# Kernel optimization log

Measured on AMD Instinct MI355X. Metric: run time of the kernel, lower is better.

Reference implementation:

```python
import jax, jax.numpy as jnp
import numpy as np

# ----- problem dimensions (must match setup_inputs) -----
B = 50          # graphs per batch
NPG = 2000      # nodes per graph (equal-size graphs)
N = B * NPG     # total nodes = 100_000
D = 128         # in_channels
E = 600_000     # total edges
EA = 16         # edge_attr_dim
RATIO = 0.5
K = int(RATIO * NPG)  # nodes kept per graph = 1000
EPS = 1e-6


def setup_inputs() -> dict:
    key = jax.random.key(0)
    ks = jax.random.split(key, 12)
    x = jax.random.normal(ks[0], (N, D), jnp.float32)
    # edges constrained within graphs (each graph owns a contiguous node block)
    eg = jax.random.randint(ks[1], (E,), 0, B)
    src = eg * NPG + jax.random.randint(ks[2], (E,), 0, NPG)
    dst = eg * NPG + jax.random.randint(ks[3], (E,), 0, NPG)
    edge_index = jnp.stack([src, dst]).astype(jnp.int32)
    edge_attr = jax.random.normal(ks[4], (E, EA), jnp.float32)
    batch = (jnp.arange(N) // NPG).astype(jnp.int32)
    # feat_mlp: Linear(D,D) -> ReLU -> Linear(D,1)
    W1 = jax.random.normal(ks[5], (D, D), jnp.float32) / np.sqrt(D)
    b1 = jnp.zeros((D,), jnp.float32)
    W2 = jax.random.normal(ks[6], (D, 1), jnp.float32) / np.sqrt(D)
    b2 = jnp.zeros((1,), jnp.float32)
    # edge_mlp: Linear(EA,D) -> ReLU -> Linear(D,1)
    We1 = jax.random.normal(ks[7], (EA, D), jnp.float32) / np.sqrt(EA)
    be1 = jnp.zeros((D,), jnp.float32)
    We2 = jax.random.normal(ks[8], (D, 1), jnp.float32) / np.sqrt(D)
    be2 = jnp.zeros((1,), jnp.float32)
    view_weight = jnp.ones((3,), jnp.float32)
    return {"x": x, "edge_index": edge_index, "edge_attr": edge_attr,
            "batch": batch, "W1": W1, "b1": b1, "W2": W2, "b2": b2,
            "We1": We1, "be1": be1, "We2": We2, "be2": be2,
            "view_weight": view_weight}


def _standardize(v):
    # torch .std() is unbiased (ddof=1)
    return (v - v.mean()) / (jnp.std(v, ddof=1) + EPS)


def _scores(x, src, dst, edge_attr, W1, b1, W2, b2, We1, be1, We2, be2, vw):
    # edge weights: softplus(edge_mlp(edge_attr)) + eps
    ew = jax.nn.softplus((jax.nn.relu(edge_attr @ We1 + be1) @ We2 + be2)[:, 0]) + EPS
    deg_w = jnp.zeros((N,), x.dtype).at[src].add(ew)
    dis = jnp.where(deg_w > 0, deg_w ** -0.5, 0.0)
    norm = dis[src] * ew * dis[dst]                       # [E]
    x_diff = jnp.zeros_like(x).at[src].add(x[dst] * norm[:, None])  # [N,D]
    # view 1: structural (log degree)
    deg_c = jnp.zeros((N,), x.dtype).at[src].add(1.0)
    struct_score = _standardize(jnp.log(deg_c + 1.0))
    # view 2: feature MLP
    feat_raw = (jax.nn.relu(x @ W1 + b1) @ W2 + b2)[:, 0]
    feat_score = _standardize(feat_raw)
    # view 3: diffusion cosine similarity
    dot = jnp.sum(x * x_diff, axis=-1)
    cos = dot / ((jnp.linalg.norm(x, axis=-1) + EPS) *
                 (jnp.linalg.norm(x_diff, axis=-1) + EPS))
    diff_score = _standardize(cos)
    raw = jnp.stack([struct_score, feat_score, diff_score], axis=-1) @ vw
    return jax.nn.sigmoid(raw)                            # [N]


def reference(x, edge_index, edge_attr, batch, W1, b1, W2, b2,
              We1, be1, We2, be2, view_weight):
    src, dst = edge_index[0], edge_index[1]
    score = _scores(x, src, dst, edge_attr, W1, b1, W2, b2,
                    We1, be1, We2, be2, view_weight)
    # vectorized per-graph top-k (graphs are equal-size contiguous blocks)
    loc = jax.lax.top_k(score.reshape(B, NPG), K)[1]      # [B,K] local indices
    keep = (jnp.arange(B, dtype=loc.dtype)[:, None] * NPG + loc).reshape(-1)  # [B*K]
    node_mask = jnp.zeros((N,), bool).at[keep].set(True)
    new_id = jnp.full((N,), -1, jnp.int32).at[keep].set(
        jnp.arange(B * K, dtype=jnp.int32))
    e_mask = node_mask[src] & node_mask[dst]              # [E]
    out_edge_index = jnp.where(e_mask[None, :],
                               jnp.stack([new_id[src], new_id[dst]]), 0)
    out_edge_attr = jnp.where(e_mask[:, None], edge_attr, 0.0)
    out_x = x[keep] * score[keep][:, None]                # [B*K, D]
    out_batch = (jnp.arange(B * K) // K).astype(batch.dtype)
    return out_x, out_edge_index, out_edge_attr, out_batch, e_mask
```

## Files before the change

kernel.cpp:

```cpp
#include <hip/hip_runtime.h>
#include <math.h>

#define NN   100000
#define DD   128
#define EE   600000
#define EAD  16
#define BB   50
#define NPG  2000
#define KK   1000
#define NKEEP (BB*KK)

#define OFF_OEI    6400000
#define OFF_OEA    7600000
#define OFF_OBATCH 17200000
#define OFF_EMASK  17250000

#define NRED 240
#define SCAN_NB 98

__global__ __launch_bounds__(256) void k_edge_mlp(
    const float* __restrict__ edge_attr, const int* __restrict__ src,
    const float* __restrict__ We1, const float* __restrict__ be1,
    const float* __restrict__ We2, const float* __restrict__ be2,
    float* __restrict__ ew, float* __restrict__ deg_w, float* __restrict__ deg_c)
{
    int e = blockIdx.x * 256 + threadIdx.x;
    if (e >= EE) return;
    const float4* ap = (const float4*)(edge_attr + (size_t)e * EAD);
    float4 a0 = ap[0], a1 = ap[1], a2 = ap[2], a3 = ap[3];
    float ea[16] = {a0.x,a0.y,a0.z,a0.w, a1.x,a1.y,a1.z,a1.w,
                    a2.x,a2.y,a2.z,a2.w, a3.x,a3.y,a3.z,a3.w};
    float acc = be2[0];
    for (int j = 0; j < DD; j++) {
        float h = be1[j];
        #pragma unroll
        for (int k = 0; k < 16; k++) h += ea[k] * We1[k*DD + j];
        acc += fmaxf(h, 0.f) * We2[j];
    }
    float sp = fmaxf(acc, 0.f) + log1pf(expf(-fabsf(acc)));
    float w = sp + 1e-6f;
    ew[e] = w;
    int s = src[e];
    atomicAdd(&deg_w[s], w);
    atomicAdd(&deg_c[s], 1.0f);
}

__global__ __launch_bounds__(256) void k_dis(const float* __restrict__ deg_w,
                                             float* __restrict__ dis)
{
    int n = blockIdx.x * 256 + threadIdx.x;
    if (n >= NN) return;
    float d = deg_w[n];
    dis[n] = d > 0.f ? 1.f / sqrtf(d) : 0.f;
}

__global__ __launch_bounds__(1024) void k_scan_block(
    const float* __restrict__ deg_c, int* __restrict__ scanned,
    int* __restrict__ blocksums)
{
    __shared__ int s[1024];
    int i = blockIdx.x * 1024 + threadIdx.x;
    int c = (i < NN) ? (int)deg_c[i] : 0;
    s[threadIdx.x] = c;
    __syncthreads();
    for (int off = 1; off < 1024; off <<= 1) {
        int v = (threadIdx.x >= off) ? s[threadIdx.x - off] : 0;
        __syncthreads();
        s[threadIdx.x] += v;
        __syncthreads();
    }
    if (i < NN) scanned[i] = s[threadIdx.x] - c;
    if (threadIdx.x == 1023) blocksums[blockIdx.x] = s[1023];
}

__global__ __launch_bounds__(128) void k_scan_top(int* __restrict__ blocksums)
{
    __shared__ int s[128];
    int c = (threadIdx.x < SCAN_NB) ? blocksums[threadIdx.x] : 0;
    s[threadIdx.x] = c;
    __syncthreads();
    for (int off = 1; off < 128; off <<= 1) {
        int v = (threadIdx.x >= off) ? s[threadIdx.x - off] : 0;
        __syncthreads();
        s[threadIdx.x] += v;
        __syncthreads();
    }
    if (threadIdx.x < SCAN_NB) blocksums[threadIdx.x] = s[threadIdx.x] - c;
}

__global__ __launch_bounds__(256) void k_cursor(
    const int* __restrict__ scanned, const int* __restrict__ blocksums,
    int* __restrict__ rowstart, int* __restrict__ cur)
{
    int n = blockIdx.x * 256 + threadIdx.x;
    if (n >= NN) return;
    int st = scanned[n] + blocksums[n >> 10];
    rowstart[n] = st;
    cur[n] = st;
}

__global__ __launch_bounds__(256) void k_scatter(
    const int* __restrict__ src, const int* __restrict__ dst,
    const float* __restrict__ ew, const float* __restrict__ dis,
    int* __restrict__ cur, int* __restrict__ csr_dst, float* __restrict__ csr_w)
{
    int e = blockIdx.x * 256 + threadIdx.x;
    if (e >= EE) return;
    int s = src[e], d = dst[e];
    float w = dis[s] * ew[e] * dis[d];
    int pos = atomicAdd(&cur[s], 1);
    csr_dst[pos] = d;
    csr_w[pos] = w;
}

__global__ __launch_bounds__(256) void k_gather(
    const int* __restrict__ rowstart, const float* __restrict__ deg_c,
    const int* __restrict__ csr_dst, const float* __restrict__ csr_w,
    const float* __restrict__ x, float* __restrict__ x_diff)
{
    int wid = (blockIdx.x * 256 + threadIdx.x) >> 6;
    int lane = threadIdx.x & 63;
    if (wid >= NN) return;
    int start = rowstart[wid];
    int end = start + (int)deg_c[wid];
    const float2* xp = (const float2*)x;
    float2 acc = {0.f, 0.f};
    for (int e = start; e < end; e++) {
        int d = csr_dst[e];
        float w = csr_w[e];
        float2 xv = xp[(size_t)d * 64 + lane];
        acc.x += xv.x * w;
        acc.y += xv.y * w;
    }
    ((float2*)x_diff)[(size_t)wid * 64 + lane] = acc;
}

#define XSTR 132
__global__ __launch_bounds__(256) void k_node(
    const float* __restrict__ x, const float* __restrict__ x_diff,
    const float* __restrict__ W1, const float* __restrict__ b1,
    const float* __restrict__ W2, const float* __restrict__ b2,
    const float* __restrict__ deg_c,
    float* __restrict__ raw0, float* __restrict__ raw1, float* __restrict__ raw2)
{
    __shared__ float xs[64 * XSTR];
    int wave = threadIdx.x >> 6, lane = threadIdx.x & 63;
    int ng = lane >> 4, jg = lane & 15;
    int blockBase = blockIdx.x * 64;

    #pragma unroll
    for (int it = 0; it < 8; it++) {
        int s = threadIdx.x + 256 * it;
        int row = s >> 5, c4 = s & 31;
        int gn = blockBase + row; if (gn >= NN) gn = NN - 1;
        *(float4*)(xs + row * XSTR + c4 * 4) =
            *(const float4*)(x + (size_t)gn * DD + c4 * 4);
    }
    __syncthreads();

    const float* xw = xs + (wave * 16 + ng * 4) * XSTR;
    int j0 = jg * 8;
    float acc[4][8];
    #pragma unroll
    for (int i = 0; i < 4; i++)
        #pragma unroll
        for (int jj = 0; jj < 8; jj++) acc[i][jj] = 0.f;

    for (int k = 0; k < DD; k += 4) {
        float4 xv[4];
        #pragma unroll
        for (int i = 0; i < 4; i++) xv[i] = *(const float4*)(xw + i * XSTR + k);
        float4 wv[4][2];
        #pragma unroll
        for (int kk = 0; kk < 4; kk++) {
            wv[kk][0] = *(const float4*)(W1 + (k + kk) * DD + j0);
            wv[kk][1] = *(const float4*)(W1 + (k + kk) * DD + j0 + 4);
        }
        #pragma unroll
        for (int i = 0; i < 4; i++) {
            const float xe[4] = {xv[i].x, xv[i].y, xv[i].z, xv[i].w};
            #pragma unroll
            for (int kk = 0; kk < 4; kk++) {
                acc[i][0] += xe[kk] * wv[kk][0].x;
                acc[i][1] += xe[kk] * wv[kk][0].y;
                acc[i][2] += xe[kk] * wv[kk][0].z;
                acc[i][3] += xe[kk] * wv[kk][0].w;
                acc[i][4] += xe[kk] * wv[kk][1].x;
                acc[i][5] += xe[kk] * wv[kk][1].y;
                acc[i][6] += xe[kk] * wv[kk][1].z;
                acc[i][7] += xe[kk] * wv[kk][1].w;
            }
        }
    }

    float4 b1a = *(const float4*)(b1 + j0), b1b = *(const float4*)(b1 + j0 + 4);
    float4 w2a = *(const float4*)(W2 + j0), w2b = *(const float4*)(W2 + j0 + 4);
    const float b1v[8] = {b1a.x,b1a.y,b1a.z,b1a.w, b1b.x,b1b.y,b1b.z,b1b.w};
    const float w2v[8] = {w2a.x,w2a.y,w2a.z,w2a.w, w2b.x,w2b.y,w2b.z,w2b.w};
    float bias2 = b2[0];
    #pragma unroll
    for (int i = 0; i < 4; i++) {
        float p = 0.f;
        #pragma unroll
        for (int jj = 0; jj < 8; jj++)
            p += fmaxf(acc[i][jj] + b1v[jj], 0.f) * w2v[jj];
        p += __shfl_xor(p, 1, 64);
        p += __shfl_xor(p, 2, 64);
        p += __shfl_xor(p, 4, 64);
        p += __shfl_xor(p, 8, 64);
        int node = blockBase + wave * 16 + ng * 4 + i;
        if (jg == 0 && node < NN) raw1[node] = p + bias2;
    }

    const float* xwv = xs + wave * 16 * XSTR;
    #pragma unroll 1
    for (int nd = 0; nd < 16; nd++) {
        int node = blockBase + wave * 16 + nd;
        int rn = node < NN ? node : NN - 1;
        float2 xv2 = *(const float2*)(xwv + nd * XSTR + lane * 2);
        float2 xd2 = *(const float2*)(x_diff + (size_t)rn * DD + lane * 2);
        float dot = xv2.x * xd2.x + xv2.y * xd2.y;
        float nx  = xv2.x * xv2.x + xv2.y * xv2.y;
        float ndn = xd2.x * xd2.x + xd2.y * xd2.y;
        #pragma unroll
        for (int off = 32; off; off >>= 1) {
            dot += __shfl_xor(dot, off, 64);
            nx  += __shfl_xor(nx,  off, 64);
            ndn += __shfl_xor(ndn, off, 64);
        }
        if (lane == 0 && node < NN)
            raw2[node] = dot / ((sqrtf(nx) + 1e-6f) * (sqrtf(ndn) + 1e-6f));
    }
    if (lane < 16) {
        int node = blockBase + wave * 16 + lane;
        if (node < NN) raw0[node] = logf(deg_c[node] + 1.0f);
    }
}

__global__ __launch_bounds__(256) void k_reduce(
    const float* __restrict__ r0, const float* __restrict__ r1,
    const float* __restrict__ r2, double* __restrict__ partials)
{
    __shared__ double sd[256];
    double s[6] = {0,0,0,0,0,0};
    for (int n = blockIdx.x * 256 + threadIdx.x; n < NN; n += 256 * NRED) {
        double v0 = r0[n], v1 = r1[n], v2 = r2[n];
        s[0] += v0; s[1] += v0*v0;
        s[2] += v1; s[3] += v1*v1;
        s[4] += v2; s[5] += v2*v2;
    }
    for (int q = 0; q < 6; q++) {
        sd[threadIdx.x] = s[q];
        __syncthreads();
        for (int off = 128; off; off >>= 1) {
            if (threadIdx.x < off) sd[threadIdx.x] += sd[threadIdx.x + off];
            __syncthreads();
        }
        if (threadIdx.x == 0) partials[blockIdx.x * 6 + q] = sd[0];
        __syncthreads();
    }
}

__global__ __launch_bounds__(256) void k_stats(const double* __restrict__ partials,
                                               float* __restrict__ stats)
{
    __shared__ double sd[256];
    __shared__ double sums[6];
    for (int q = 0; q < 6; q++) {
        sd[threadIdx.x] = (threadIdx.x < NRED) ? partials[threadIdx.x * 6 + q] : 0.0;
        __syncthreads();
        for (int off = 128; off; off >>= 1) {
            if (threadIdx.x < off) sd[threadIdx.x] += sd[threadIdx.x + off];
            __syncthreads();
        }
        if (threadIdx.x == 0) sums[q] = sd[0];
        __syncthreads();
    }
    if (threadIdx.x == 0) {
        for (int i = 0; i < 3; i++) {
            double sum = sums[2*i], sq = sums[2*i+1];
            double mean = sum / NN;
            double var = (sq - sum * sum / NN) / (NN - 1);
            double sdv = sqrt(var > 0 ? var : 0);
            stats[2*i]   = (float)mean;
            stats[2*i+1] = (float)(1.0 / (sdv + 1e-6));
        }
    }
}

__global__ __launch_bounds__(256) void k_score(
    const float* __restrict__ r0, const float* __restrict__ r1,
    const float* __restrict__ r2, const float* __restrict__ stats,
    const float* __restrict__ vw, float* __restrict__ score)
{
    int n = blockIdx.x * 256 + threadIdx.x;
    if (n >= NN) return;
    float z0 = (r0[n] - stats[0]) * stats[1];
    float z1 = (r1[n] - stats[2]) * stats[3];
    float z2 = (r2[n] - stats[4]) * stats[5];
    float r = z0 * vw[0] + z1 * vw[1] + z2 * vw[2];
    score[n] = 1.f / (1.f + expf(-r));
}

__global__ __launch_bounds__(1024) void k_topk(
    const float* __restrict__ score, int* __restrict__ keep,
    int* __restrict__ new_id, float* __restrict__ obatch)
{
    __shared__ unsigned long long keys[2048];
    int b = blockIdx.x;
    unsigned t = threadIdx.x;
    for (unsigned i = t; i < 2048; i += 1024) {
        unsigned long long kk = 0ull;
        if (i < NPG) {
            float sc = score[b * NPG + i];
            kk = ((unsigned long long)__float_as_uint(sc) << 32)
               | (unsigned long long)(0xFFFFFFFFu - i);
        }
        keys[i] = kk;
    }
    __syncthreads();
    for (unsigned k = 2; k <= 2048; k <<= 1) {
        for (unsigned j = k >> 1; j > 0; j >>= 1) {
            unsigned i = ((t & ~(j - 1)) << 1) | (t & (j - 1));
            unsigned p = i | j;
            unsigned long long a = keys[i], c = keys[p];
            bool up = ((i & k) == 0);
            if ((a < c) == up) { keys[i] = c; keys[p] = a; }
            __syncthreads();
        }
    }
    if (t < KK) {
        unsigned long long kk = keys[t];
        unsigned li = 0xFFFFFFFFu - (unsigned)(kk & 0xFFFFFFFFu);
        int node = b * NPG + (int)li;
        int j = b * KK + (int)t;
        keep[j] = node;
        new_id[node] = j;
        obatch[j] = (float)b;
    }
}

__global__ __launch_bounds__(128) void k_outx(
    const float* __restrict__ x, const float* __restrict__ score,
    const int* __restrict__ keep, float* __restrict__ out_x)
{
    int j = blockIdx.x;
    int node = keep[j];
    float s = score[node];
    out_x[(size_t)j * DD + threadIdx.x] = x[(size_t)node * DD + threadIdx.x] * s;
}

__global__ __launch_bounds__(256) void k_edges(
    const int* __restrict__ src, const int* __restrict__ dst,
    const int* __restrict__ new_id, float* __restrict__ oei,
    float* __restrict__ emask)
{
    int e = blockIdx.x * 256 + threadIdx.x;
    if (e >= EE) return;
    int ns = new_id[src[e]], nd = new_id[dst[e]];
    bool m = (ns >= 0) && (nd >= 0);
    oei[e]      = m ? (float)ns : 0.f;
    oei[EE + e] = m ? (float)nd : 0.f;
    emask[e]    = m ? 1.f : 0.f;
}

__global__ __launch_bounds__(256) void k_attr(
    const float* __restrict__ edge_attr, const float* __restrict__ emask,
    float* __restrict__ oea)
{
    int idx = blockIdx.x * 256 + threadIdx.x;
    if (idx >= EE * 4) return;
    int e = idx >> 2;
    float m = emask[e];
    float4 v = ((const float4*)edge_attr)[idx];
    float4 o; o.x = v.x*m; o.y = v.y*m; o.z = v.z*m; o.w = v.w*m;
    ((float4*)oea)[idx] = o;
}

extern "C" void kernel_launch(void* const* d_in, const int* in_sizes, int n_in,
                              void* d_out, int out_size, void* d_ws, size_t ws_size,
                              hipStream_t stream) {
    const float* x         = (const float*)d_in[0];
    const int*   edge_idx  = (const int*)d_in[1];
    const float* edge_attr = (const float*)d_in[2];
    const float* W1  = (const float*)d_in[4];
    const float* b1  = (const float*)d_in[5];
    const float* W2  = (const float*)d_in[6];
    const float* b2  = (const float*)d_in[7];
    const float* We1 = (const float*)d_in[8];
    const float* be1 = (const float*)d_in[9];
    const float* We2 = (const float*)d_in[10];
    const float* be2 = (const float*)d_in[11];
    const float* vw  = (const float*)d_in[12];

    const int* src = edge_idx;
    const int* dst = edge_idx + EE;

    float* out    = (float*)d_out;
    float* out_x  = out;
    float* oei    = out + OFF_OEI;
    float* oea    = out + OFF_OEA;
    float* obatch = out + OFF_OBATCH;
    float* emask  = out + OFF_EMASK;

    float* x_diff    = out;
    int*   csr_dst   = (int*)(out + 12800000);
    float* csr_w     = out + 13400000;
    int*   rowstart  = (int*)(out + 14000000);
    int*   cur       = (int*)(out + 14100000);
    int*   scanned   = (int*)(out + 14200000);
    int*   blocksums = (int*)(out + 14300000);

    float* ws     = (float*)d_ws;
    float* ew     = ws;
    float* deg_w  = ws + 600000;
    float* deg_c  = ws + 700000;
    float* dis    = ws + 800000;
    float* score  = ws + 900000;
    float* raw0   = ws + 1000000;
    float* raw1   = ws + 1100000;
    float* raw2   = ws + 1200000;
    int*   keep   = (int*)(ws + 1300000);
    int*   new_id = (int*)(ws + 1350000);
    double* partials = (double*)(ws + 1450000);
    float* stats  = ws + 1450000 + 2 * 6 * NRED;

    hipMemsetAsync(deg_w, 0, 2 * NN * sizeof(float), stream);
    hipMemsetAsync(new_id, 0xFF, NN * sizeof(int), stream);

    k_edge_mlp<<<(EE + 255) / 256, 256, 0, stream>>>(edge_attr, src, We1, be1, We2, be2,
                                                     ew, deg_w, deg_c);
    k_dis<<<(NN + 255) / 256, 256, 0, stream>>>(deg_w, dis);
    k_scan_block<<<SCAN_NB, 1024, 0, stream>>>(deg_c, scanned, blocksums);
    k_scan_top<<<1, 128, 0, stream>>>(blocksums);
    k_cursor<<<(NN + 255) / 256, 256, 0, stream>>>(scanned, blocksums, rowstart, cur);
    k_scatter<<<(EE + 255) / 256, 256, 0, stream>>>(src, dst, ew, dis, cur, csr_dst, csr_w);
    k_gather<<<(NN * 64 + 255) / 256, 256, 0, stream>>>(rowstart, deg_c, csr_dst, csr_w,
                                                        x, x_diff);
    k_node<<<(NN + 63) / 64, 256, 0, stream>>>(x, x_diff, W1, b1, W2, b2, deg_c,
                                               raw0, raw1, raw2);
    k_reduce<<<NRED, 256, 0, stream>>>(raw0, raw1, raw2, partials);
    k_stats<<<1, 256, 0, stream>>>(partials, stats);
    k_score<<<(NN + 255) / 256, 256, 0, stream>>>(raw0, raw1, raw2, stats, vw, score);
    k_topk<<<BB, 1024, 0, stream>>>(score, keep, new_id, obatch);
    k_outx<<<NKEEP, 128, 0, stream>>>(x, score, keep, out_x);
    k_edges<<<(EE + 255) / 256, 256, 0, stream>>>(src, dst, new_id, oei, emask);
    k_attr<<<(EE * 4 + 255) / 256, 256, 0, stream>>>(edge_attr, emask, oea);
}
```

Measured before the change: 512.5 us.

## Fuse cosine similarity into neighbor gather and tile edge MLP weights in LDS

The edge MLP kernel now stages a transposed copy of We1, be1 and We2 in shared memory and has each thread process four edges, reusing each weight load across them. The neighbor gather now computes the cosine-similarity and log-degree features directly, so the x_diff array is never written to memory or read back in the node kernel. The gather also loads CSR indices and weights cooperatively across the wavefront and broadcasts them with shuffles, unrolled four at a time for more memory parallelism. The edge kernel gains register pressure and launches fewer blocks.

```diff
diff --git a/kernel.cpp b/kernel.cpp
--- a/kernel.cpp
+++ b/kernel.cpp
@@ -18,31 +18,73 @@
 #define NRED 240
 #define SCAN_NB 98
 
+#define EPB 1024
 __global__ __launch_bounds__(256) void k_edge_mlp(
     const float* __restrict__ edge_attr, const int* __restrict__ src,
     const float* __restrict__ We1, const float* __restrict__ be1,
     const float* __restrict__ We2, const float* __restrict__ be2,
     float* __restrict__ ew, float* __restrict__ deg_w, float* __restrict__ deg_c)
 {
-    int e = blockIdx.x * 256 + threadIdx.x;
-    if (e >= EE) return;
-    const float4* ap = (const float4*)(edge_attr + (size_t)e * EAD);
-    float4 a0 = ap[0], a1 = ap[1], a2 = ap[2], a3 = ap[3];
-    float ea[16] = {a0.x,a0.y,a0.z,a0.w, a1.x,a1.y,a1.z,a1.w,
-                    a2.x,a2.y,a2.z,a2.w, a3.x,a3.y,a3.z,a3.w};
-    float acc = be2[0];
+    __shared__ float wt[2048];
+    __shared__ float b1s[128];
+    __shared__ float w2s[128];
+    for (int idx = threadIdx.x; idx < 2048; idx += 256) {
+        int j = idx >> 4, k = idx & 15;
+        wt[idx] = We1[k * DD + j];
+    }
+    if (threadIdx.x < 128) {
+        b1s[threadIdx.x] = be1[threadIdx.x];
+        w2s[threadIdx.x] = We2[threadIdx.x];
+    }
+    __syncthreads();
+
+    int e0 = blockIdx.x * EPB + threadIdx.x;
+    float ea[4][16];
+    #pragma unroll
+    for (int i = 0; i < 4; i++) {
+        int e = e0 + 256 * i; if (e >= EE) e = EE - 1;
+        const float4* ap = (const float4*)(edge_attr + (size_t)e * EAD);
+        float4 a0 = ap[0], a1 = ap[1], a2 = ap[2], a3 = ap[3];
+        ea[i][0]=a0.x; ea[i][1]=a0.y; ea[i][2]=a0.z; ea[i][3]=a0.w;
+        ea[i][4]=a1.x; ea[i][5]=a1.y; ea[i][6]=a1.z; ea[i][7]=a1.w;
+        ea[i][8]=a2.x; ea[i][9]=a2.y; ea[i][10]=a2.z; ea[i][11]=a2.w;
+        ea[i][12]=a3.x; ea[i][13]=a3.y; ea[i][14]=a3.z; ea[i][15]=a3.w;
+    }
+    float acc[4] = {0.f, 0.f, 0.f, 0.f};
     for (int j = 0; j < DD; j++) {
-        float h = be1[j];
-        #pragma unroll
-        for (int k = 0; k < 16; k++) h += ea[k] * We1[k*DD + j];
-        acc += fmaxf(h, 0.f) * We2[j];
-    }
-    float sp = fmaxf(acc, 0.f) + log1pf(expf(-fabsf(acc)));
-    float w = sp + 1e-6f;
-    ew[e] = w;
-    int s = src[e];
-    atomicAdd(&deg_w[s], w);
-    atomicAdd(&deg_c[s], 1.0f);
+        float4 w0 = *(const float4*)(wt + j*16);
+        float4 w1 = *(const float4*)(wt + j*16 + 4);
+        float4 w2 = *(const float4*)(wt + j*16 + 8);
+        float4 w3 = *(const float4*)(wt + j*16 + 12);
+        float bj = b1s[j], w2j = w2s[j];
+        #pragma unroll
+        for (int i = 0; i < 4; i++) {
+            float h = bj;
+            h += ea[i][0]*w0.x;  h += ea[i][1]*w0.y;
+            h += ea[i][2]*w0.z;  h += ea[i][3]*w0.w;
+            h += ea[i][4]*w1.x;  h += ea[i][5]*w1.y;
+            h += ea[i][6]*w1.z;  h += ea[i][7]*w1.w;
+            h += ea[i][8]*w2.x;  h += ea[i][9]*w2.y;
+            h += ea[i][10]*w2.z; h += ea[i][11]*w2.w;
+            h += ea[i][12]*w3.x; h += ea[i][13]*w3.y;
+            h += ea[i][14]*w3.z; h += ea[i][15]*w3.w;
+            acc[i] += fmaxf(h, 0.f) * w2j;
+        }
+    }
+    float bias2 = be2[0];
+    #pragma unroll
+    for (int i = 0; i < 4; i++) {
+        int e = e0 + 256 * i;
+        if (e < EE) {
+            float a = acc[i] + bias2;
+            float sp = fmaxf(a, 0.f) + log1pf(expf(-fabsf(a)));
+            float w = sp + 1e-6f;
+            ew[e] = w;
+            int s = src[e];
+            atomicAdd(&deg_w[s], w);
+            atomicAdd(&deg_c[s], 1.0f);
+        }
+    }
 }
 
 __global__ __launch_bounds__(256) void k_dis(const float* __restrict__ deg_w,
@@ -113,35 +155,69 @@
     csr_w[pos] = w;
 }
 
-__global__ __launch_bounds__(256) void k_gather(
+__global__ __launch_bounds__(256) void k_gather_cos(
     const int* __restrict__ rowstart, const float* __restrict__ deg_c,
     const int* __restrict__ csr_dst, const float* __restrict__ csr_w,
-    const float* __restrict__ x, float* __restrict__ x_diff)
-{
-    int wid = (blockIdx.x * 256 + threadIdx.x) >> 6;
+    const float* __restrict__ x, float* __restrict__ raw0, float* __restrict__ raw2)
+{
+    int node = (blockIdx.x * 256 + threadIdx.x) >> 6;
     int lane = threadIdx.x & 63;
-    if (wid >= NN) return;
-    int start = rowstart[wid];
-    int end = start + (int)deg_c[wid];
+    if (node >= NN) return;
+    int start = rowstart[node];
+    int deg = (int)deg_c[node];
     const float2* xp = (const float2*)x;
+    float2 xn = xp[(size_t)node * 64 + lane];
     float2 acc = {0.f, 0.f};
-    for (int e = start; e < end; e++) {
-        int d = csr_dst[e];
-        float w = csr_w[e];
-        float2 xv = xp[(size_t)d * 64 + lane];
-        acc.x += xv.x * w;
-        acc.y += xv.y * w;
-    }
-    ((float2*)x_diff)[(size_t)wid * 64 + lane] = acc;
+    for (int base = 0; base < deg; base += 64) {
+        int rem = deg - base; if (rem > 64) rem = 64;
+        int md = 0; float mw = 0.f;
+        if (lane < rem) {
+            md = csr_dst[start + base + lane];
+            mw = csr_w[start + base + lane];
+        }
+        int e = 0;
+        for (; e + 4 <= rem; e += 4) {
+            int d0 = __shfl(md, e, 64),   d1 = __shfl(md, e+1, 64);
+            int d2 = __shfl(md, e+2, 64), d3 = __shfl(md, e+3, 64);
+            float w0 = __shfl(mw, e, 64),   w1 = __shfl(mw, e+1, 64);
+            float w2 = __shfl(mw, e+2, 64), w3 = __shfl(mw, e+3, 64);
+            float2 v0 = xp[(size_t)d0 * 64 + lane];
+            float2 v1 = xp[(size_t)d1 * 64 + lane];
+            float2 v2 = xp[(size_t)d2 * 64 + lane];
+            float2 v3 = xp[(size_t)d3 * 64 + lane];
+            acc.x += w0 * v0.x; acc.y += w0 * v0.y;
+            acc.x += w1 * v1.x; acc.y += w1 * v1.y;
+            acc.x += w2 * v2.x; acc.y += w2 * v2.y;
+            acc.x += w3 * v3.x; acc.y += w3 * v3.y;
+        }
+        for (; e < rem; e++) {
+            int d = __shfl(md, e, 64);
+            float w = __shfl(mw, e, 64);
+            float2 v = xp[(size_t)d * 64 + lane];
+            acc.x += w * v.x; acc.y += w * v.y;
+        }
+    }
+    float dot = xn.x * acc.x + xn.y * acc.y;
+    float nx  = xn.x * xn.x + xn.y * xn.y;
+    float nd  = acc.x * acc.x + acc.y * acc.y;
+    #pragma unroll
+    for (int off = 32; off; off >>= 1) {
+        dot += __shfl_xor(dot, off, 64);
+        nx  += __shfl_xor(nx,  off, 64);
+        nd  += __shfl_xor(nd,  off, 64);
+    }
+    if (lane == 0) {
+        raw2[node] = dot / ((sqrtf(nx) + 1e-6f) * (sqrtf(nd) + 1e-6f));
+        raw0[node] = logf((float)deg + 1.0f);
+    }
 }
 
 #define XSTR 132
 __global__ __launch_bounds__(256) void k_node(
-    const float* __restrict__ x, const float* __restrict__ x_diff,
+    const float* __restrict__ x,
     const float* __restrict__ W1, const float* __restrict__ b1,
     const float* __restrict__ W2, const float* __restrict__ b2,
-    const float* __restrict__ deg_c,
-    float* __restrict__ raw0, float* __restrict__ raw1, float* __restrict__ raw2)
+    float* __restrict__ raw1)
 {
     __shared__ float xs[64 * XSTR];
     int wave = threadIdx.x >> 6, lane = threadIdx.x & 63;
@@ -210,30 +286,6 @@
         p += __shfl_xor(p, 8, 64);
         int node = blockBase + wave * 16 + ng * 4 + i;
         if (jg == 0 && node < NN) raw1[node] = p + bias2;
-    }
-
-    const float* xwv = xs + wave * 16 * XSTR;
-    #pragma unroll 1
-    for (int nd = 0; nd < 16; nd++) {
-        int node = blockBase + wave * 16 + nd;
-        int rn = node < NN ? node : NN - 1;
-        float2 xv2 = *(const float2*)(xwv + nd * XSTR + lane * 2);
-        float2 xd2 = *(const float2*)(x_diff + (size_t)rn * DD + lane * 2);
-        float dot = xv2.x * xd2.x + xv2.y * xd2.y;
-        float nx  = xv2.x * xv2.x + xv2.y * xv2.y;
-        float ndn = xd2.x * xd2.x + xd2.y * xd2.y;
-        #pragma unroll
-        for (int off = 32; off; off >>= 1) {
-            dot += __shfl_xor(dot, off, 64);
-            nx  += __shfl_xor(nx,  off, 64);
-            ndn += __shfl_xor(ndn, off, 64);
-        }
-        if (lane == 0 && node < NN)
-            raw2[node] = dot / ((sqrtf(nx) + 1e-6f) * (sqrtf(ndn) + 1e-6f));
-    }
-    if (lane < 16) {
-        int node = blockBase + wave * 16 + lane;
-        if (node < NN) raw0[node] = logf(deg_c[node] + 1.0f);
     }
 }
 
@@ -403,7 +455,6 @@
     float* obatch = out + OFF_OBATCH;
     float* emask  = out + OFF_EMASK;
 
-    float* x_diff    = out;
     int*   csr_dst   = (int*)(out + 12800000);
     float* csr_w     = out + 13400000;
     int*   rowstart  = (int*)(out + 14000000);
@@ -428,17 +479,16 @@
     hipMemsetAsync(deg_w, 0, 2 * NN * sizeof(float), stream);
     hipMemsetAsync(new_id, 0xFF, NN * sizeof(int), stream);
 
-    k_edge_mlp<<<(EE + 255) / 256, 256, 0, stream>>>(edge_attr, src, We1, be1, We2, be2,
-                                                     ew, deg_w, deg_c);
+    k_edge_mlp<<<(EE + EPB - 1) / EPB, 256, 0, stream>>>(edge_attr, src, We1, be1,
+                                                         We2, be2, ew, deg_w, deg_c);
     k_dis<<<(NN + 255) / 256, 256, 0, stream>>>(deg_w, dis);
     k_scan_block<<<SCAN_NB, 1024, 0, stream>>>(deg_c, scanned, blocksums);
     k_scan_top<<<1, 128, 0, stream>>>(blocksums);
     k_cursor<<<(NN + 255) / 256, 256, 0, stream>>>(scanned, blocksums, rowstart, cur);
     k_scatter<<<(EE + 255) / 256, 256, 0, stream>>>(src, dst, ew, dis, cur, csr_dst, csr_w);
-    k_gather<<<(NN * 64 + 255) / 256, 256, 0, stream>>>(rowstart, deg_c, csr_dst, csr_w,
-                                                        x, x_diff);
-    k_node<<<(NN + 63) / 64, 256, 0, stream>>>(x, x_diff, W1, b1, W2, b2, deg_c,
-                                               raw0, raw1, raw2);
+    k_gather_cos<<<(NN * 64 + 255) / 256, 256, 0, stream>>>(rowstart, deg_c, csr_dst,
+                                                            csr_w, x, raw0, raw2);
+    k_node<<<(NN + 63) / 64, 256, 0, stream>>>(x, W1, b1, W2, b2, raw1);
     k_reduce<<<NRED, 256, 0, stream>>>(raw0, raw1, raw2, partials);
     k_stats<<<1, 256, 0, stream>>>(partials, stats);
     k_score<<<(NN + 255) / 256, 256, 0, stream>>>(raw0, raw1, raw2, stats, vw, score);
```

Result: faster. 452.6 us (-11.7%).
